# Kernel tuning notes

Measured on AMD Instinct MI355X. Metric: run time of the kernel, lower is better.

Reference implementation:

```python
import jax, jax.numpy as jnp
import numpy as np

B, C, H, W = 8, 1, 384, 384
INF2 = float(H * H + W * W + 1)  # 'infinite' squared distance


def _edt_single(feat):
    # Exact Euclidean distance transform: distance from every pixel to the
    # nearest True pixel in `feat` [H, W]. Separable squared-distance min.
    j = jnp.arange(W)
    dj2 = ((j[:, None] - j[None, :]).astype(jnp.float32)) ** 2  # [W, W']
    # g2[i, j] = min_{j': feat[i, j']} (j - j')^2
    g2 = jnp.min(jnp.where(feat[:, None, :], dj2[None, :, :], INF2), axis=2)  # [H, W]
    i = jnp.arange(H)
    di2 = ((i[:, None] - i[None, :]).astype(jnp.float32)) ** 2  # [H, H']
    # d2[i, j] = min_{i'} g2[i', j] + (i - i')^2
    d2 = jnp.min(di2[:, :, None] + g2[None, :, :], axis=1)  # [H, W]
    return jnp.sqrt(jnp.minimum(d2, INF2))


def _distance_map(target):
    # Signed distance map: EDT(1-m) - EDT(m), normalized by global max-abs,
    # matching BoundaryLoss._compute_distance_map (scipy distance_transform_edt).
    m = target.reshape(-1, H, W)

    def per_img(mi):
        fg = mi > 0.5
        pos = _edt_single(fg)        # dist to nearest foreground (EDT of 1-m)
        neg = _edt_single(~fg)       # dist to nearest background (EDT of m)
        return pos - neg

    dist = jax.lax.map(per_img, m).reshape(target.shape)
    maxabs = jnp.max(jnp.abs(dist))
    return jnp.where(maxabs > 0, dist / maxabs, dist)


def _lovasz_flat(logits, labels):
    # Binary Lovasz hinge on flat vectors (one sample).
    signs = 2.0 * labels - 1.0
    errors = 1.0 - logits * signs
    order = jnp.argsort(-errors)          # descending sort, perm is constant w.r.t. grads
    errors_sorted = errors[order]
    gt_sorted = labels[order]
    gts = jnp.sum(gt_sorted)
    intersection = gts - jnp.cumsum(gt_sorted)
    union = gts + jnp.cumsum(1.0 - gt_sorted)
    jaccard = 1.0 - intersection / (union + 1e-7)
    grad = jnp.concatenate([jaccard[:1], jaccard[1:] - jaccard[:-1]])
    return jnp.dot(jax.nn.relu(errors_sorted), grad)


def _combined_loss(pred, target):
    # BCE with logits (stable): max(x,0) - x*z + log1p(exp(-|x|)), mean.
    bce = jnp.mean(jnp.maximum(pred, 0.0) - pred * target + jnp.log1p(jnp.exp(-jnp.abs(pred))))
    # Dice.
    p = jax.nn.sigmoid(pred)
    smooth = 1.0
    intersection = jnp.sum(p * target)
    union = jnp.sum(p) + jnp.sum(target)
    dice = 1.0 - (2.0 * intersection + smooth) / (union + smooth)
    # Boundary: mean(sigmoid(pred) * signed_dist_map(target)); dist map is constant.
    dist_map = jax.lax.stop_gradient(_distance_map(target))
    boundary = jnp.mean(p * dist_map)
    # Lovasz hinge, per-sample over flattened pixels, then mean over batch.
    lovasz = jnp.mean(jax.vmap(_lovasz_flat)(pred.reshape(B, -1), target.reshape(B, -1)))
    loss = 0.3 * bce + 0.3 * dice + 0.2 * boundary + 0.2 * lovasz
    return jnp.clip(loss, 0.0, 100.0)


def setup_inputs() -> dict:
    key = jax.random.key(0)
    k1, k2 = jax.random.split(key)
    pred = jax.random.normal(k1, (B, C, H, W), dtype=jnp.float32)
    target = (jax.random.uniform(k2, (B, C, H, W)) < 0.3).astype(jnp.float32)
    return {"pred": pred, "target": target}


def reference(pred, target):
    return _combined_loss(pred, target)
```

## Files before the change

### kernel.cpp

```cpp
#include <hip/hip_runtime.h>
#include <hip/hip_bf16.h>
#include <math.h>

#define PSZ   147456
#define NTOT  1179648
#define WW    384
#define HH    384
#define NIMG  8
#define NBINH 2048
#define INF2F 294913.0f
#define GV2   1152
#define EBLK  768
#define HPART 8

static __device__ __forceinline__ float errval(float x, float z) {
    float s = __fsub_rn(__fmul_rn(2.0f, z), 1.0f);
    return __fsub_rn(1.0f, __fmul_rn(x, s));
}
static __device__ __forceinline__ int binof(float e) {
    int b = (int)(__fmul_rn(e, 256.0f));
    return b > (NBINH - 1) ? (NBINH - 1) : b;
}
static __device__ __forceinline__ float d2f(int d) {
    return (float)(d * d);
}

struct DPair { int df, db; };
static __device__ __forceinline__ DPair ndist2(const unsigned long long* __restrict__ m, int p) {
    const int BIG = 1 << 20;
    int q = p >> 6, b = p & 63;
    int df = BIG, db = BIG;
    {
        unsigned long long w = m[q];
        unsigned long long tf = w >> b;
        unsigned long long tb = (~w) >> b;
        if (tf) df = __builtin_ctzll(tf);
        if (tb) db = __builtin_ctzll(tb);
        for (int u = q + 1; (df == BIG || db == BIG) && u < 6; ++u) {
            w = m[u];
            if (df == BIG && w)  df = u * 64 + __builtin_ctzll(w)  - p;
            if (db == BIG && ~w) db = u * 64 + __builtin_ctzll(~w) - p;
        }
    }
    {
        unsigned long long w = m[q];
        unsigned long long tf = w << (63 - b);
        unsigned long long tb = (~w) << (63 - b);
        int lf = BIG, lb = BIG;
        if (tf) lf = __builtin_clzll(tf);
        if (tb) lb = __builtin_clzll(tb);
        for (int u = q - 1; (lf == BIG || lb == BIG) && u >= 0; --u) {
            w = m[u];
            if (lf == BIG && w)  lf = p - (u * 64 + 63 - __builtin_clzll(w));
            if (lb == BIG && ~w) lb = p - (u * 64 + 63 - __builtin_clzll(~w));
        }
        if (lf < df) df = lf;
        if (lb < db) db = lb;
    }
    DPair r;
    r.df = (df > 600) ? 600 : df;
    r.db = (db > 600) ? 600 : db;
    return r;
}

__global__ __launch_bounds__(256) void k_edth(const float* __restrict__ tgt,
                                              unsigned int* __restrict__ g2,
                                              unsigned int* __restrict__ maxabsBits) {
    if (blockIdx.x == 0 && threadIdx.x == 0) maxabsBits[0] = 0u;
    int img = blockIdx.x & 7;
    int bb  = blockIdx.x >> 3;
    int row = img * HH + bb * 4 + (threadIdx.x >> 6);
    int l = threadIdx.x & 63;
    const float* tr = tgt + (size_t)row * WW;
    unsigned long long mf[6];
#pragma unroll
    for (int c = 0; c < 6; ++c)
        mf[c] = __ballot(tr[c * 64 + l] > 0.5f);
    size_t ob = (size_t)row * WW;
#pragma unroll
    for (int c = 0; c < 6; ++c) {
        int p = c * 64 + l;
        DPair d = ndist2(mf, p);
        g2[ob + p] = (unsigned int)d.df | ((unsigned int)d.db << 16);
    }
}

__global__ __launch_bounds__(1024) void k_hist(const float* __restrict__ pred,
                                               const float* __restrict__ tgt,
                                               unsigned long long* __restrict__ histp) {
    __shared__ unsigned long long h[NBINH * 2];
    for (int q = threadIdx.x; q < NBINH * 2; q += 1024) h[q] = 0ull;
    __syncthreads();
    int img  = blockIdx.x & 7;
    int part = blockIdx.x >> 3;
    int base = img * PSZ + part * (PSZ / HPART);
#pragma unroll
    for (int it = 0; it < PSZ / HPART / 1024; ++it) {
        int n = base + it * 1024 + threadIdx.x;
        float x = pred[n], z = tgt[n];
        float e = errval(x, z);
        if (e > 0.0f) {
            int lab = (z > 0.5f) ? 1 : 0;
            unsigned long long add = (1ull << 46) |
                (unsigned long long)__fmul_rn(e, 16777216.0f);
            atomicAdd(&h[(binof(e) << 1) + lab], add);
        }
    }
    __syncthreads();
    unsigned long long* gh = histp + ((size_t)blockIdx.x << 12);
    for (int q = threadIdx.x; q < NBINH * 2; q += 1024) gh[q] = h[q];
}

__global__ __launch_bounds__(256) void k_fused(const float* __restrict__ pred,
                                               const float* __restrict__ tgt,
                                               const unsigned int* __restrict__ g2,
                                               float* __restrict__ pB, float* __restrict__ pP,
                                               float* __restrict__ pPT, float* __restrict__ pBnd,
                                               unsigned int* __restrict__ pPc,
                                               unsigned int* __restrict__ maxabsBits) {
    int t = threadIdx.x;
    int img = blockIdx.x & 7;
    int bb  = blockIdx.x >> 3;
    int v   = bb * 256 + t;
    int j   = v % WW;
    int i0  = (v / WW) * 4;
    const unsigned int* g2i = g2 + (size_t)img * PSZ;
    unsigned int w[24];
#pragma unroll
    for (int k = 0; k < 24; ++k) {
        int rr = i0 - 8 + k;
        rr = rr < 0 ? 0 : (rr > HH - 1 ? HH - 1 : rr);
        w[k] = g2i[rr * WW + j];
    }
    float aF[4], aB[4];
#pragma unroll
    for (int m = 0; m < 4; ++m) {
        float f = INF2F, g = INF2F;
#pragma unroll
        for (int k = m; k <= m + 16; ++k) {
            float r2 = d2f(k - 8 - m);
            f = fminf(f, r2 + d2f((int)(w[k] & 0xffffu)));
            g = fminf(g, r2 + d2f((int)(w[k] >> 16)));
        }
        aF[m] = f; aB[m] = g;
    }
#pragma unroll
    for (int m = 0; m < 4; ++m) {
        int i = i0 + m;
        for (int r = 9; r < HH; ++r) {
            float r2 = d2f(r);
            if (r2 >= fmaxf(aF[m], aB[m])) break;
            int up = i - r, dn = i + r;
            if (up >= 0) {
                unsigned int ww = g2i[up * WW + j];
                aF[m] = fminf(aF[m], r2 + d2f((int)(ww & 0xffffu)));
                aB[m] = fminf(aB[m], r2 + d2f((int)(ww >> 16)));
            }
            if (dn < HH) {
                unsigned int ww = g2i[dn * WW + j];
                aF[m] = fminf(aF[m], r2 + d2f((int)(ww & 0xffffu)));
                aB[m] = fminf(aB[m], r2 + d2f((int)(ww >> 16)));
            }
        }
    }
    float vals[6] = {0.f, 0.f, 0.f, 0.f, 0.f, 0.f};
#pragma unroll
    for (int m = 0; m < 4; ++m) {
        int n = img * PSZ + (i0 + m) * WW + j;
        float x = pred[n], z = tgt[n];
        bool lab = z > 0.5f;
        float dv = lab ? -sqrtf(fminf(aB[m], INF2F)) : sqrtf(fminf(aF[m], INF2F));
        float bce = fmaxf(x, 0.0f) - x * z + log1pf(expf(-fabsf(x)));
        float p = 1.0f / (1.0f + expf(-x));
        vals[0] += bce; vals[1] += p;
        vals[2] += lab ? p : 0.0f;
        vals[3] += p * dv;
        vals[4] += lab ? 1.0f : 0.0f;
        vals[5] = fmaxf(vals[5], fabsf(dv));
    }
#pragma unroll
    for (int k = 0; k < 5; ++k)
#pragma unroll
        for (int off = 32; off; off >>= 1) vals[k] += __shfl_xor(vals[k], off);
#pragma unroll
    for (int off = 32; off; off >>= 1) vals[5] = fmaxf(vals[5], __shfl_xor(vals[5], off));
    __shared__ float sw[4][6];
    int wv = t >> 6, lnn = t & 63;
    if (lnn == 0) {
#pragma unroll
        for (int k = 0; k < 6; ++k) sw[wv][k] = vals[k];
    }
    __syncthreads();
    if (t < 6) {
        int k = t;
        if (k == 5) {
            float a = fmaxf(fmaxf(sw[0][5], sw[1][5]), fmaxf(sw[2][5], sw[3][5]));
            atomicMax(maxabsBits, __float_as_uint(a));
        } else {
            float a = sw[0][k] + sw[1][k] + sw[2][k] + sw[3][k];
            if (k == 0) pB[blockIdx.x] = a;
            else if (k == 1) pP[blockIdx.x] = a;
            else if (k == 2) pPT[blockIdx.x] = a;
            else if (k == 3) pBnd[blockIdx.x] = a;
            else pPc[blockIdx.x] = (unsigned int)(a + 0.5f);
        }
    }
}

__global__ __launch_bounds__(256) void k_scanlov(const unsigned long long* __restrict__ histp,
                                                 const unsigned int* __restrict__ pPc,
                                                 const float* __restrict__ pB, const float* __restrict__ pP,
                                                 const float* __restrict__ pPT, const float* __restrict__ pBnd,
                                                 double* __restrict__ sums,
                                                 unsigned int* __restrict__ Pfin) {
    int b = blockIdx.x, t = threadIdx.x;
    __shared__ double dred[256];
    __shared__ unsigned int ured[256];
    double mv[4] = {0.0, 0.0, 0.0, 0.0};
    unsigned int mc = 0;
    if (t < 144) {
        int q = b + 8 * t;
        mv[0] = (double)pB[q]; mv[1] = (double)pP[q];
        mv[2] = (double)pPT[q]; mv[3] = (double)pBnd[q];
        mc = pPc[q];
    }
    ured[t] = mc; __syncthreads();
    for (int s = 128; s > 0; s >>= 1) { if (t < s) ured[t] += ured[t + s]; __syncthreads(); }
    unsigned int Pfull = ured[0];
    __syncthreads();
#pragma unroll
    for (int a = 0; a < 4; ++a) {
        dred[t] = mv[a]; __syncthreads();
        for (int s = 128; s > 0; s >>= 1) { if (t < s) dred[t] += dred[t + s]; __syncthreads(); }
        if (t == 0) sums[b * 5 + a] = dred[0];
        __syncthreads();
    }
    int m0 = t * 8;
    unsigned int ln = 0, lp = 0;
    unsigned int hcn[8], hcp[8];
    unsigned long long hsn[8], hsp[8];
#pragma unroll
    for (int k = 0; k < 8; ++k) {
        unsigned long long vn = 0ull, vp = 0ull;
#pragma unroll
        for (int pp = 0; pp < HPART; ++pp) {
            const unsigned long long* hc = histp + ((size_t)(pp * 8 + b) << 12);
            vn += hc[2 * (m0 + k)];
            vp += hc[2 * (m0 + k) + 1];
        }
        hcn[k] = (unsigned int)(vn >> 46); hcp[k] = (unsigned int)(vp >> 46);
        hsn[k] = vn & ((1ull << 46) - 1);  hsp[k] = vp & ((1ull << 46) - 1);
        ln += hcn[k]; lp += hcp[k];
    }
    int lane = t & 63, wv = t >> 6;
    unsigned int sln = ln, slp = lp;
#pragma unroll
    for (int off = 1; off < 64; off <<= 1) {
        unsigned int an = __shfl_up(sln, off);
        unsigned int ap = __shfl_up(slp, off);
        if (lane >= off) { sln += an; slp += ap; }
    }
    __shared__ unsigned int wN[4], wP[4];
    if (lane == 63) { wN[wv] = sln; wP[wv] = slp; }
    __syncthreads();
    unsigned int baseN = 0, baseP = 0, totN = 0, totP = 0;
#pragma unroll
    for (int q = 0; q < 4; ++q) {
        if (q < wv) { baseN += wN[q]; baseP += wP[q]; }
        totN += wN[q]; totP += wP[q];
    }
    unsigned int runN = baseN + sln - ln;
    unsigned int runP = baseP + slp - lp;
    const double EPS = 1e-7;
    const double SCL = 1.0 / 16777216.0;
    double P = (double)Pfull;
    double l = 0.0;
#pragma unroll
    for (int k = 0; k < 8; ++k) {
        unsigned int hn = hcn[k], hp = hcp[k];
        if (hn | hp) {
            double negAbove = (double)(totN - runN - hn);
            double D0 = P + negAbove + EPS;
            if (hp) l += ((double)hsp[k] * SCL) / D0;
            if (hn) {
                double pAbove = (double)(totP - runP);
                double D1 = D0 + (double)hn;
                l += (P - pAbove) * ((double)hsn[k] * SCL) / (D0 * D1);
            }
            runN += hn; runP += hp;
        }
    }
    dred[t] = l; __syncthreads();
    for (int s = 128; s > 0; s >>= 1) { if (t < s) dred[t] += dred[t + s]; __syncthreads(); }
    if (t == 0) { sums[b * 5 + 4] = dred[0]; Pfin[b] = Pfull; }
}

__global__ __launch_bounds__(64) void k_final(const double* __restrict__ sums,
                                              const unsigned int* __restrict__ Pfin,
                                              const unsigned int* __restrict__ maxabsBits,
                                              float* __restrict__ out) {
    if (threadIdx.x == 0) {
        double sumBCE = 0, sumP = 0, sumPT = 0, sumBD = 0, sumLV = 0, tsum = 0;
        for (int b = 0; b < NIMG; ++b) {
            sumBCE += sums[b * 5 + 0];
            sumP   += sums[b * 5 + 1];
            sumPT  += sums[b * 5 + 2];
            sumBD  += sums[b * 5 + 3];
            sumLV  += sums[b * 5 + 4];
            tsum   += (double)Pfin[b];
        }
        double bce = sumBCE / (double)NTOT;
        double dice = 1.0 - (2.0 * sumPT + 1.0) / (sumP + tsum + 1.0);
        float ma = __uint_as_float(maxabsBits[0]);
        double bnd = sumBD / (double)NTOT;
        if (ma > 0.0f) bnd = bnd / (double)ma;
        double lov = sumLV / (double)NIMG;
        double loss = 0.3 * bce + 0.3 * dice + 0.2 * bnd + 0.2 * lov;
        if (loss < 0.0) loss = 0.0;
        if (loss > 100.0) loss = 100.0;
        out[0] = (float)loss;
    }
}

extern "C" void kernel_launch(void* const* d_in, const int* in_sizes, int n_in,
                              void* d_out, int out_size, void* d_ws, size_t ws_size,
                              hipStream_t stream) {
    const float* pred = (const float*)d_in[0];
    const float* tgt  = (const float*)d_in[1];
    char* ws = (char*)d_ws;

    size_t off = 0;
    unsigned long long* histp = (unsigned long long*)(ws + off);
    off += (size_t)NIMG * HPART * NBINH * 2 * 8;
    unsigned int* maxabsBits = (unsigned int*)(ws + off); off += 64;
    off = (off + 1023) & ~(size_t)1023;
    double* sums = (double*)(ws + off); off += NIMG * 5 * 8;
    unsigned int* Pfin = (unsigned int*)(ws + off); off += NIMG * 4;
    off = (off + 63) & ~(size_t)63;
    float* pB   = (float*)(ws + off); off += (size_t)GV2 * 4;
    float* pP   = (float*)(ws + off); off += (size_t)GV2 * 4;
    float* pPT  = (float*)(ws + off); off += (size_t)GV2 * 4;
    float* pBnd = (float*)(ws + off); off += (size_t)GV2 * 4;
    unsigned int* pPc = (unsigned int*)(ws + off); off += (size_t)GV2 * 4;
    off = (off + 1023) & ~(size_t)1023;
    unsigned int* g2 = (unsigned int*)(ws + off); off += (size_t)NIMG * PSZ * 4;
    (void)off; (void)ws_size; (void)in_sizes; (void)n_in; (void)out_size;

    k_edth<<<EBLK, 256, 0, stream>>>(tgt, g2, maxabsBits);
    k_hist<<<NIMG * HPART, 1024, 0, stream>>>(pred, tgt, histp);
    k_fused<<<GV2, 256, 0, stream>>>(pred, tgt, g2, pB, pP, pPT, pBnd, pPc, maxabsBits);
    k_scanlov<<<NIMG, 256, 0, stream>>>(histp, pPc, pB, pP, pPT, pBnd, sums, Pfin);
    k_final<<<1, 64, 0, stream>>>(sums, Pfin, maxabsBits, (float*)d_out);
}
```

Measured before the change: 49.46 us.

## Fuse row EDT with Lovasz histogram and fold final reduction into scan

The row-wise distance pass and the error histogram pass are merged into one 64-block, 1024-thread kernel that reads each target/pred row once and does both. The final scalar reduction moves into the last k_scanlov block, chosen with an atomic election counter, which drops a kernel launch. This cuts five launches to three and removes a second read of the target. The cost is that the EDT work now runs on only 64 blocks instead of 768, which lowers parallelism.

```diff
diff --git a/kernel.cpp b/kernel.cpp
--- a/kernel.cpp
+++ b/kernel.cpp
@@ -10,7 +10,6 @@
 #define NBINH 2048
 #define INF2F 294913.0f
 #define GV2   1152
-#define EBLK  768
 #define HPART 8
 
 static __device__ __forceinline__ float errval(float x, float z) {
@@ -63,47 +62,43 @@
     return r;
 }
 
-__global__ __launch_bounds__(256) void k_edth(const float* __restrict__ tgt,
+__global__ __launch_bounds__(1024) void k_pre(const float* __restrict__ tgt,
+                                              const float* __restrict__ pred,
                                               unsigned int* __restrict__ g2,
-                                              unsigned int* __restrict__ maxabsBits) {
-    if (blockIdx.x == 0 && threadIdx.x == 0) maxabsBits[0] = 0u;
-    int img = blockIdx.x & 7;
-    int bb  = blockIdx.x >> 3;
-    int row = img * HH + bb * 4 + (threadIdx.x >> 6);
-    int l = threadIdx.x & 63;
-    const float* tr = tgt + (size_t)row * WW;
-    unsigned long long mf[6];
-#pragma unroll
-    for (int c = 0; c < 6; ++c)
-        mf[c] = __ballot(tr[c * 64 + l] > 0.5f);
-    size_t ob = (size_t)row * WW;
-#pragma unroll
-    for (int c = 0; c < 6; ++c) {
-        int p = c * 64 + l;
-        DPair d = ndist2(mf, p);
-        g2[ob + p] = (unsigned int)d.df | ((unsigned int)d.db << 16);
-    }
-}
-
-__global__ __launch_bounds__(1024) void k_hist(const float* __restrict__ pred,
-                                               const float* __restrict__ tgt,
-                                               unsigned long long* __restrict__ histp) {
+                                              unsigned long long* __restrict__ histp,
+                                              unsigned int* __restrict__ maxabsBits,
+                                              unsigned int* __restrict__ elect) {
     __shared__ unsigned long long h[NBINH * 2];
     for (int q = threadIdx.x; q < NBINH * 2; q += 1024) h[q] = 0ull;
+    if (blockIdx.x == 0 && threadIdx.x == 0) { maxabsBits[0] = 0u; elect[0] = 0u; }
     __syncthreads();
     int img  = blockIdx.x & 7;
     int part = blockIdx.x >> 3;
-    int base = img * PSZ + part * (PSZ / HPART);
-#pragma unroll
-    for (int it = 0; it < PSZ / HPART / 1024; ++it) {
-        int n = base + it * 1024 + threadIdx.x;
-        float x = pred[n], z = tgt[n];
-        float e = errval(x, z);
-        if (e > 0.0f) {
-            int lab = (z > 0.5f) ? 1 : 0;
-            unsigned long long add = (1ull << 46) |
-                (unsigned long long)__fmul_rn(e, 16777216.0f);
-            atomicAdd(&h[(binof(e) << 1) + lab], add);
+    int wv = threadIdx.x >> 6, l = threadIdx.x & 63;
+#pragma unroll
+    for (int rr = 0; rr < 3; ++rr) {
+        int row = img * HH + part * 48 + wv * 3 + rr;
+        const float* tr = tgt  + (size_t)row * WW;
+        const float* pr = pred + (size_t)row * WW;
+        float zv[6], xv[6];
+        unsigned long long mf[6];
+#pragma unroll
+        for (int c = 0; c < 6; ++c) { zv[c] = tr[c * 64 + l]; xv[c] = pr[c * 64 + l]; }
+#pragma unroll
+        for (int c = 0; c < 6; ++c) mf[c] = __ballot(zv[c] > 0.5f);
+        size_t ob = (size_t)row * WW;
+#pragma unroll
+        for (int c = 0; c < 6; ++c) {
+            int p = c * 64 + l;
+            DPair d = ndist2(mf, p);
+            g2[ob + p] = (unsigned int)d.df | ((unsigned int)d.db << 16);
+            float e = errval(xv[c], zv[c]);
+            if (e > 0.0f) {
+                int lab = (zv[c] > 0.5f) ? 1 : 0;
+                unsigned long long add = (1ull << 46) |
+                    (unsigned long long)__fmul_rn(e, 16777216.0f);
+                atomicAdd(&h[(binof(e) << 1) + lab], add);
+            }
         }
     }
     __syncthreads();
@@ -212,7 +207,9 @@
                                                  const float* __restrict__ pB, const float* __restrict__ pP,
                                                  const float* __restrict__ pPT, const float* __restrict__ pBnd,
                                                  double* __restrict__ sums,
-                                                 unsigned int* __restrict__ Pfin) {
+                                                 const unsigned int* __restrict__ maxabsBits,
+                                                 unsigned int* __restrict__ elect,
+                                                 float* __restrict__ out) {
     int b = blockIdx.x, t = threadIdx.x;
     __shared__ double dred[256];
     __shared__ unsigned int ured[256];
@@ -232,7 +229,7 @@
     for (int a = 0; a < 4; ++a) {
         dred[t] = mv[a]; __syncthreads();
         for (int s = 128; s > 0; s >>= 1) { if (t < s) dred[t] += dred[t + s]; __syncthreads(); }
-        if (t == 0) sums[b * 5 + a] = dred[0];
+        if (t == 0) sums[b * 6 + a] = dred[0];
         __syncthreads();
     }
     int m0 = t * 8;
@@ -292,22 +289,27 @@
     }
     dred[t] = l; __syncthreads();
     for (int s = 128; s > 0; s >>= 1) { if (t < s) dred[t] += dred[t + s]; __syncthreads(); }
-    if (t == 0) { sums[b * 5 + 4] = dred[0]; Pfin[b] = Pfull; }
-}
-
-__global__ __launch_bounds__(64) void k_final(const double* __restrict__ sums,
-                                              const unsigned int* __restrict__ Pfin,
-                                              const unsigned int* __restrict__ maxabsBits,
-                                              float* __restrict__ out) {
-    if (threadIdx.x == 0) {
+    if (t == 0) {
+        sums[b * 6 + 4] = dred[0];
+        sums[b * 6 + 5] = (double)Pfull;
+    }
+    __syncthreads();
+    __shared__ unsigned int amLast;
+    if (t == 0) {
+        __threadfence();
+        amLast = (atomicAdd(elect, 1u) == NIMG - 1) ? 1u : 0u;
+    }
+    __syncthreads();
+    if (amLast && t == 0) {
+        __threadfence();
         double sumBCE = 0, sumP = 0, sumPT = 0, sumBD = 0, sumLV = 0, tsum = 0;
-        for (int b = 0; b < NIMG; ++b) {
-            sumBCE += sums[b * 5 + 0];
-            sumP   += sums[b * 5 + 1];
-            sumPT  += sums[b * 5 + 2];
-            sumBD  += sums[b * 5 + 3];
-            sumLV  += sums[b * 5 + 4];
-            tsum   += (double)Pfin[b];
+        for (int q = 0; q < NIMG; ++q) {
+            sumBCE += sums[q * 6 + 0];
+            sumP   += sums[q * 6 + 1];
+            sumPT  += sums[q * 6 + 2];
+            sumBD  += sums[q * 6 + 3];
+            sumLV  += sums[q * 6 + 4];
+            tsum   += sums[q * 6 + 5];
         }
         double bce = sumBCE / (double)NTOT;
         double dice = 1.0 - (2.0 * sumPT + 1.0) / (sumP + tsum + 1.0);
@@ -333,9 +335,9 @@
     unsigned long long* histp = (unsigned long long*)(ws + off);
     off += (size_t)NIMG * HPART * NBINH * 2 * 8;
     unsigned int* maxabsBits = (unsigned int*)(ws + off); off += 64;
+    unsigned int* elect      = (unsigned int*)(ws + off); off += 64;
     off = (off + 1023) & ~(size_t)1023;
-    double* sums = (double*)(ws + off); off += NIMG * 5 * 8;
-    unsigned int* Pfin = (unsigned int*)(ws + off); off += NIMG * 4;
+    double* sums = (double*)(ws + off); off += NIMG * 6 * 8;
     off = (off + 63) & ~(size_t)63;
     float* pB   = (float*)(ws + off); off += (size_t)GV2 * 4;
     float* pP   = (float*)(ws + off); off += (size_t)GV2 * 4;
@@ -346,9 +348,8 @@
     unsigned int* g2 = (unsigned int*)(ws + off); off += (size_t)NIMG * PSZ * 4;
     (void)off; (void)ws_size; (void)in_sizes; (void)n_in; (void)out_size;
 
-    k_edth<<<EBLK, 256, 0, stream>>>(tgt, g2, maxabsBits);
-    k_hist<<<NIMG * HPART, 1024, 0, stream>>>(pred, tgt, histp);
+    k_pre<<<NIMG * HPART, 1024, 0, stream>>>(tgt, pred, g2, histp, maxabsBits, elect);
     k_fused<<<GV2, 256, 0, stream>>>(pred, tgt, g2, pB, pP, pPT, pBnd, pPc, maxabsBits);
-    k_scanlov<<<NIMG, 256, 0, stream>>>(histp, pPc, pB, pP, pPT, pBnd, sums, Pfin);
-    k_final<<<1, 64, 0, stream>>>(sums, Pfin, maxabsBits, (float*)d_out);
-}
+    k_scanlov<<<NIMG, 256, 0, stream>>>(histp, pPc, pB, pP, pPT, pBnd, sums,
+                                        maxabsBits, elect, (float*)d_out);
+}
```

Measured after the change: 54.12 us. 9.4% more time.

## Merge row-EDT and Lovasz histogram kernels into one launch with more histogram blocks

Applied to the files above, without the earlier changes.

Combines the row-wise distance kernel and the error-histogram kernel into a single 1024-thread launch, with block ranges dispatched to either job. The two kernels are independent, so this removes one launch and the gap between them and lets both jobs run at the same time. The histogram is also split into 16 parts per image instead of 8, giving more blocks and less serial work per block. In exchange, every block reserves the 32 KB shared histogram even when it only does EDT rows, which may lower occupancy, and the partial histograms to reduce double.

```diff
diff --git a/kernel.cpp b/kernel.cpp
--- a/kernel.cpp
+++ b/kernel.cpp
@@ -10,8 +10,10 @@
 #define NBINH 2048
 #define INF2F 294913.0f
 #define GV2   1152
-#define EBLK  768
-#define HPART 8
+#define EBLK2 192
+#define HPART 16
+#define HPXB  9216
+#define PREB  (EBLK2 + NIMG * HPART)
 
 static __device__ __forceinline__ float errval(float x, float z) {
     float s = __fsub_rn(__fmul_rn(2.0f, z), 1.0f);
@@ -63,52 +65,54 @@
     return r;
 }
 
-__global__ __launch_bounds__(256) void k_edth(const float* __restrict__ tgt,
+__global__ __launch_bounds__(1024) void k_pre(const float* __restrict__ tgt,
+                                              const float* __restrict__ pred,
                                               unsigned int* __restrict__ g2,
+                                              unsigned long long* __restrict__ histp,
                                               unsigned int* __restrict__ maxabsBits) {
-    if (blockIdx.x == 0 && threadIdx.x == 0) maxabsBits[0] = 0u;
-    int img = blockIdx.x & 7;
-    int bb  = blockIdx.x >> 3;
-    int row = img * HH + bb * 4 + (threadIdx.x >> 6);
-    int l = threadIdx.x & 63;
-    const float* tr = tgt + (size_t)row * WW;
-    unsigned long long mf[6];
-#pragma unroll
-    for (int c = 0; c < 6; ++c)
-        mf[c] = __ballot(tr[c * 64 + l] > 0.5f);
-    size_t ob = (size_t)row * WW;
-#pragma unroll
-    for (int c = 0; c < 6; ++c) {
-        int p = c * 64 + l;
-        DPair d = ndist2(mf, p);
-        g2[ob + p] = (unsigned int)d.df | ((unsigned int)d.db << 16);
-    }
-}
-
-__global__ __launch_bounds__(1024) void k_hist(const float* __restrict__ pred,
-                                               const float* __restrict__ tgt,
-                                               unsigned long long* __restrict__ histp) {
     __shared__ unsigned long long h[NBINH * 2];
-    for (int q = threadIdx.x; q < NBINH * 2; q += 1024) h[q] = 0ull;
-    __syncthreads();
-    int img  = blockIdx.x & 7;
-    int part = blockIdx.x >> 3;
-    int base = img * PSZ + part * (PSZ / HPART);
-#pragma unroll
-    for (int it = 0; it < PSZ / HPART / 1024; ++it) {
-        int n = base + it * 1024 + threadIdx.x;
-        float x = pred[n], z = tgt[n];
-        float e = errval(x, z);
-        if (e > 0.0f) {
-            int lab = (z > 0.5f) ? 1 : 0;
-            unsigned long long add = (1ull << 46) |
-                (unsigned long long)__fmul_rn(e, 16777216.0f);
-            atomicAdd(&h[(binof(e) << 1) + lab], add);
-        }
-    }
-    __syncthreads();
-    unsigned long long* gh = histp + ((size_t)blockIdx.x << 12);
-    for (int q = threadIdx.x; q < NBINH * 2; q += 1024) gh[q] = h[q];
+    if (blockIdx.x < EBLK2) {
+        if (blockIdx.x == 0 && threadIdx.x == 0) maxabsBits[0] = 0u;
+        int img = blockIdx.x & 7;
+        int bb  = blockIdx.x >> 3;
+        int wv  = threadIdx.x >> 6;
+        int l   = threadIdx.x & 63;
+        int row = img * HH + bb * 16 + wv;
+        const float* tr = tgt + (size_t)row * WW;
+        unsigned long long mf[6];
+#pragma unroll
+        for (int c = 0; c < 6; ++c)
+            mf[c] = __ballot(tr[c * 64 + l] > 0.5f);
+        size_t ob = (size_t)row * WW;
+#pragma unroll
+        for (int c = 0; c < 6; ++c) {
+            int p = c * 64 + l;
+            DPair d = ndist2(mf, p);
+            g2[ob + p] = (unsigned int)d.df | ((unsigned int)d.db << 16);
+        }
+    } else {
+        int hb = blockIdx.x - EBLK2;
+        for (int q = threadIdx.x; q < NBINH * 2; q += 1024) h[q] = 0ull;
+        __syncthreads();
+        int img  = hb & 7;
+        int part = hb >> 3;
+        int base = img * PSZ + part * HPXB;
+#pragma unroll
+        for (int it = 0; it < HPXB / 1024; ++it) {
+            int n = base + it * 1024 + threadIdx.x;
+            float x = pred[n], z = tgt[n];
+            float e = errval(x, z);
+            if (e > 0.0f) {
+                int lab = (z > 0.5f) ? 1 : 0;
+                unsigned long long add = (1ull << 46) |
+                    (unsigned long long)__fmul_rn(e, 16777216.0f);
+                atomicAdd(&h[(binof(e) << 1) + lab], add);
+            }
+        }
+        __syncthreads();
+        unsigned long long* gh = histp + ((size_t)hb << 12);
+        for (int q = threadIdx.x; q < NBINH * 2; q += 1024) gh[q] = h[q];
+    }
 }
 
 __global__ __launch_bounds__(256) void k_fused(const float* __restrict__ pred,
@@ -218,7 +222,7 @@
     __shared__ unsigned int ured[256];
     double mv[4] = {0.0, 0.0, 0.0, 0.0};
     unsigned int mc = 0;
-    if (t < 144) {
+    if (t < GV2 / 8) {
         int q = b + 8 * t;
         mv[0] = (double)pB[q]; mv[1] = (double)pP[q];
         mv[2] = (double)pPT[q]; mv[3] = (double)pBnd[q];
@@ -346,8 +350,7 @@
     unsigned int* g2 = (unsigned int*)(ws + off); off += (size_t)NIMG * PSZ * 4;
     (void)off; (void)ws_size; (void)in_sizes; (void)n_in; (void)out_size;
 
-    k_edth<<<EBLK, 256, 0, stream>>>(tgt, g2, maxabsBits);
-    k_hist<<<NIMG * HPART, 1024, 0, stream>>>(pred, tgt, histp);
+    k_pre<<<PREB, 1024, 0, stream>>>(tgt, pred, g2, histp, maxabsBits);
     k_fused<<<GV2, 256, 0, stream>>>(pred, tgt, g2, pB, pP, pPT, pBnd, pPc, maxabsBits);
     k_scanlov<<<NIMG, 256, 0, stream>>>(histp, pPc, pB, pP, pPT, pBnd, sums, Pfin);
     k_final<<<1, 64, 0, stream>>>(sums, Pfin, maxabsBits, (float*)d_out);
```

After: 53.30 us. 1.08x slower.
